# Performance work log

Measured on AMD Instinct MI355X. Metric: run time of the kernel, lower is better.

Reference implementation:

```python
import jax, jax.numpy as jnp
import numpy as np

B, S, H = 2, 2048, 1024
NH, NKV, HD = 16, 4, 64
G, R = NKV, NH // NKV  # 4 kv groups, 4 query heads per group


def setup_inputs() -> dict:
    key = jax.random.key(0)
    ks = jax.random.split(key, 7)
    scale = 1.0 / np.sqrt(H)
    return {
        "hidden_states": jax.random.normal(ks[0], (B, S, H), jnp.float32),
        "cos": jax.random.normal(ks[1], (S, HD), jnp.float32),
        "sin": jax.random.normal(ks[2], (S, HD), jnp.float32),
        "attention_mask": jnp.ones((B, S), jnp.float32),
        "Wq": jax.random.normal(ks[3], (H, NH * HD), jnp.float32) * scale,
        "Wk": jax.random.normal(ks[4], (H, NKV * HD), jnp.float32) * scale,
        "Wv": jax.random.normal(ks[5], (H, NKV * HD), jnp.float32) * scale,
        "Wo": jax.random.normal(ks[6], (NH * HD, H), jnp.float32) * scale,
    }


def _rotate_half(x):
    h = x.shape[-1] // 2
    return jnp.concatenate([-x[..., h:], x[..., :h]], axis=-1)


def reference(hidden_states, cos, sin, attention_mask, Wq, Wk, Wv, Wo):
    x = hidden_states
    q = (x @ Wq).reshape(B, S, NH, HD)
    k = (x @ Wk).reshape(B, S, NKV, HD)
    v = (x @ Wv).reshape(B, S, NKV, HD)
    # RoPE: cos/sin [S,HD] broadcast over batch and heads
    c = cos[None, :, None, :]
    s = sin[None, :, None, :]
    q = q * c + _rotate_half(q) * s
    k = k * c + _rotate_half(k) * s
    # GQA without materializing repeated KV: q grouped as [B,S,G,R,HD]
    qg = q.reshape(B, S, G, R, HD)
    scores = jnp.einsum("bsgrd,btgd->bgrst", qg, k) / np.sqrt(HD)  # [B,G,R,S,T]
    causal = jnp.tril(jnp.ones((S, S), bool))
    scores = jnp.where(causal[None, None, None], scores, -jnp.inf)
    scores = scores + ((1.0 - attention_mask) * -1e9)[:, None, None, None, :]
    probs = jax.nn.softmax(scores.astype(jnp.float32), axis=-1).astype(q.dtype)
    out = jnp.einsum("bgrst,btgd->bsgrd", probs, v).reshape(B, S, NH * HD)
    return out @ Wo
```

## Files before the change

### kernel.cpp

```cpp
#include <hip/hip_runtime.h>
#include <math.h>

#define B_   2
#define S_   2048
#define H_   1024
#define NH_  16
#define NKV_ 4
#define HD_  64
#define R_   (NH_ / NKV_)
#define QKVW 1536

typedef __attribute__((ext_vector_type(8))) short bf16x8;
typedef __attribute__((ext_vector_type(4))) float f32x4;

__device__ inline short f2bf(float f) {
    unsigned u = __float_as_uint(f);
    u += 0x7FFF + ((u >> 16) & 1);
    return (short)(u >> 16);
}

__device__ inline float exp2fast(float x) {
#if __has_builtin(__builtin_amdgcn_exp2f)
    return __builtin_amdgcn_exp2f(x);
#else
    float r; asm volatile("v_exp_f32 %0, %1\n\ts_nop 1" : "=v"(r) : "v"(x)); return r;
#endif
}

__device__ inline unsigned cvt_pk_bf16(float lo, float hi) {
    unsigned r;
    asm("v_cvt_pk_bf16_f32 %0, %1, %2" : "=v"(r) : "v"(lo), "v"(hi));
    return r;
}

#define LOG2E 1.4426950408889634f

__device__ inline void gload_lds16(const void* gptr, void* lptr) {
    __builtin_amdgcn_global_load_lds(
        (const __attribute__((address_space(1))) unsigned int*)gptr,
        (__attribute__((address_space(3))) unsigned int*)lptr,
        16, 0, 0);
}

__global__ __launch_bounds__(256) void tconv_all(const float* __restrict__ Wq,
                                                 const float* __restrict__ Wk,
                                                 const float* __restrict__ Wv,
                                                 const float* __restrict__ Wo,
                                                 short* __restrict__ Wqkvt,
                                                 short* __restrict__ Wot,
                                                 const float* __restrict__ x,
                                                 short* __restrict__ xb) {
    const int bx = blockIdx.x;
    const int tid = threadIdx.x;

    if (bx >= 640) {
        const size_t e0 = (size_t)(bx - 640) * 16384;
#pragma unroll
        for (int t = 0; t < 8; t++) {
            const size_t i = e0 + ((size_t)t * 256 + tid) * 8;
            float4 a = *(const float4*)&x[i];
            float4 c = *(const float4*)&x[i + 4];
            bf16x8 o;
            o[0] = f2bf(a.x); o[1] = f2bf(a.y); o[2] = f2bf(a.z); o[3] = f2bf(a.w);
            o[4] = f2bf(c.x); o[5] = f2bf(c.y); o[6] = f2bf(c.z); o[7] = f2bf(c.w);
            *(bf16x8*)&xb[i] = o;
        }
        return;
    }

    __shared__ short T[64][68];
    const float* W; short* Wt; int N, idx;
    if (bx < 256)      { W = Wq; Wt = Wqkvt;                     N = 1024; idx = bx; }
    else if (bx < 320) { W = Wk; Wt = Wqkvt + 1024 * 1024;       N = 256;  idx = bx - 256; }
    else if (bx < 384) { W = Wv; Wt = Wqkvt + 1280 * 1024;       N = 256;  idx = bx - 320; }
    else               { W = Wo; Wt = Wot;                       N = 1024; idx = bx - 384; }
    const int ntiles = N >> 6;
    const int n0 = (idx % ntiles) * 64;
    const int k0 = (idx / ntiles) * 64;

    const int r  = tid >> 4;
    const int c4 = (tid & 15) * 4;
#pragma unroll
    for (int t = 0; t < 4; t++) {
        int row = t * 16 + r;
        float4 v = *(const float4*)&W[(size_t)(k0 + row) * N + n0 + c4];
        T[c4 + 0][row] = f2bf(v.x);
        T[c4 + 1][row] = f2bf(v.y);
        T[c4 + 2][row] = f2bf(v.z);
        T[c4 + 3][row] = f2bf(v.w);
    }
    __syncthreads();
#pragma unroll
    for (int t = 0; t < 4; t++) {
        int row = t * 16 + r;
        short4 o = *(short4*)&T[row][c4];
        *(short4*)&Wt[(size_t)(n0 + row) * 1024 + k0 + c4] = o;
    }
}

__global__ __launch_bounds__(256) void gemm1_fused(const short* __restrict__ xb,
                                                   const short* __restrict__ Bt,
                                                   short* __restrict__ qkv,
                                                   short* __restrict__ Vtg,
                                                   const float* __restrict__ cosb,
                                                   const float* __restrict__ sinb) {
    __shared__ short Ah[64 * 32];
    __shared__ short Bh[128 * 32];

    const int tid  = threadIdx.x;
    const int w    = tid >> 6;
    const int lane = tid & 63;
    const int ln   = lane & 15;
    const int qd   = lane >> 4;
    const int wr   = w >> 1, wc = w & 1;
    const int row0 = blockIdx.y * 64;
    const int col0 = blockIdx.x * 128;

    const int sr = lane >> 2;
    const int sk = (lane & 3) * 8;

    f32x4 acc[2][4];
#pragma unroll
    for (int mi = 0; mi < 2; mi++)
#pragma unroll
        for (int ni = 0; ni < 4; ni++)
            acc[mi][ni] = (f32x4){0.f, 0.f, 0.f, 0.f};

    for (int k0 = 0; k0 < 1024; k0 += 32) {
        __syncthreads();
        gload_lds16(xb + (size_t)(row0 + w * 16 + sr) * 1024 + k0 + sk,      &Ah[(w * 16) * 32]);
        gload_lds16(Bt + (size_t)(col0 + w * 32 + sr) * 1024 + k0 + sk,      &Bh[(w * 32) * 32]);
        gload_lds16(Bt + (size_t)(col0 + w * 32 + 16 + sr) * 1024 + k0 + sk, &Bh[(w * 32 + 16) * 32]);
        __syncthreads();

        bf16x8 af[2], bfr[4];
#pragma unroll
        for (int mi = 0; mi < 2; mi++)
            af[mi] = *(const bf16x8*)&Ah[(wr * 32 + mi * 16 + ln) * 32 + qd * 8];
#pragma unroll
        for (int ni = 0; ni < 4; ni++)
            bfr[ni] = *(const bf16x8*)&Bh[(wc * 64 + ni * 16 + ln) * 32 + qd * 8];
#pragma unroll
        for (int mi = 0; mi < 2; mi++)
#pragma unroll
            for (int ni = 0; ni < 4; ni++)
                acc[mi][ni] = __builtin_amdgcn_mfma_f32_16x16x32_bf16(af[mi], bfr[ni], acc[mi][ni], 0, 0, 0);
    }

    const int colw = col0 + wc * 64;
    if (colw < H_ + NKV_ * HD_) {
#pragma unroll
        for (int mi = 0; mi < 2; mi++)
#pragma unroll
            for (int i = 0; i < 4; i++) {
                const int row  = row0 + wr * 32 + mi * 16 + qd * 4 + i;
                const int spos = row & (S_ - 1);
                const float* cp = cosb + (size_t)spos * HD_;
                const float* sp = sinb + (size_t)spos * HD_;
                float o0[4];
#pragma unroll
                for (int ni = 0; ni < 2; ni++) {
                    const int d = ni * 16 + ln;
                    float x0 = acc[mi][ni][i], x1 = acc[mi][ni + 2][i];
                    o0[ni]     = x0 * cp[d]      - x1 * sp[d];
                    o0[ni + 2] = x1 * cp[d + 32] + x0 * sp[d + 32];
                }
                short* Cp = qkv + (size_t)row * QKVW + colw + ln;
#pragma unroll
                for (int ni = 0; ni < 4; ni++) Cp[ni * 16] = f2bf(o0[ni]);
            }
    } else {
        const int g = (colw - (H_ + NKV_ * HD_)) >> 6;
#pragma unroll
        for (int mi = 0; mi < 2; mi++) {
            const int rbase = row0 + wr * 32 + mi * 16 + qd * 4;
            const int bg = ((rbase >> 11) * NKV_) + g;
            const int s0 = rbase & (S_ - 1);
#pragma unroll
            for (int ni = 0; ni < 4; ni++) {
                const int d = ni * 16 + ln;
                short4 pk = { f2bf(acc[mi][ni][0]), f2bf(acc[mi][ni][1]),
                              f2bf(acc[mi][ni][2]), f2bf(acc[mi][ni][3]) };
                *(short4*)&Vtg[((size_t)bg * HD_ + d) * S_ + s0] = pk;
            }
        }
    }
}

__global__ __launch_bounds__(256) void gemm2_bt(const short* __restrict__ A, int lda,
                                                const short* __restrict__ Bt,
                                                float* __restrict__ C, int ldc,
                                                int K) {
    __shared__ short Ah[64 * 32];
    __shared__ short Bh[128 * 32];

    const int tid  = threadIdx.x;
    const int w    = tid >> 6;
    const int lane = tid & 63;
    const int ln   = lane & 15;
    const int qd   = lane >> 4;
    const int wr   = w >> 1, wc = w & 1;
    const int row0 = blockIdx.y * 64;
    const int col0 = blockIdx.x * 128;

    const int sr = lane >> 2;
    const int sk = (lane & 3) * 8;

    f32x4 acc[2][4];
#pragma unroll
    for (int mi = 0; mi < 2; mi++)
#pragma unroll
        for (int ni = 0; ni < 4; ni++)
            acc[mi][ni] = (f32x4){0.f, 0.f, 0.f, 0.f};

    for (int k0 = 0; k0 < K; k0 += 32) {
        __syncthreads();
        gload_lds16(A + (size_t)(row0 + w * 16 + sr) * lda + k0 + sk, &Ah[(w * 16) * 32]);
        gload_lds16(Bt + (size_t)(col0 + w * 32 + sr) * K + k0 + sk, &Bh[(w * 32) * 32]);
        gload_lds16(Bt + (size_t)(col0 + w * 32 + 16 + sr) * K + k0 + sk, &Bh[(w * 32 + 16) * 32]);
        __syncthreads();

        bf16x8 af[2], bfr[4];
#pragma unroll
        for (int mi = 0; mi < 2; mi++)
            af[mi] = *(const bf16x8*)&Ah[(wr * 32 + mi * 16 + ln) * 32 + qd * 8];
#pragma unroll
        for (int ni = 0; ni < 4; ni++)
            bfr[ni] = *(const bf16x8*)&Bh[(wc * 64 + ni * 16 + ln) * 32 + qd * 8];
#pragma unroll
        for (int mi = 0; mi < 2; mi++)
#pragma unroll
            for (int ni = 0; ni < 4; ni++)
                acc[mi][ni] = __builtin_amdgcn_mfma_f32_16x16x32_bf16(af[mi], bfr[ni], acc[mi][ni], 0, 0, 0);
    }

#pragma unroll
    for (int mi = 0; mi < 2; mi++)
#pragma unroll
        for (int i = 0; i < 4; i++) {
            const size_t row = row0 + wr * 32 + mi * 16 + qd * 4 + i;
            float* Cp = C + row * ldc + col0 + wc * 64 + ln;
#pragma unroll
            for (int ni = 0; ni < 4; ni++) Cp[ni * 16] = acc[mi][ni][i];
        }
}

__global__ __launch_bounds__(512, 2) void attn_kernel(short* __restrict__ qkv,
                                                      const short* __restrict__ Vtg,
                                                      const float* __restrict__ maskb) {
    const int tid  = threadIdx.x;
    const int w    = tid >> 6;
    const int lane = tid & 63;
    const int ln   = lane & 15;
    const int qd   = lane >> 4;

    const int fid = blockIdx.x;
    const int bg  = fid & 7;
    const int u   = fid >> 3;
    const int b   = bg >> 2;
    const int g   = bg & 3;
    const int h   = g * R_ + (u & 3);
    const int a   = u >> 2;

    __shared__ short Ks[2][64 * 72];
    __shared__ short Vt[2][64 * 72];
    __shared__ short Ps[8][16 * 72];
    __shared__ float mskS[2][64];
    short* const ps = Ps[w];

    const short* const Kb = qkv + (size_t)b * S_ * QKVW + H_ + g * HD_;
    const short* const Vb = Vtg + (size_t)bg * HD_ * S_;
    const float* const mb = maskb + b * S_;

    const int fr = tid >> 3;
    const int fc = (tid & 7) * 8;

#pragma unroll 1
    for (int ph = 0; ph < 2; ph++) {
        const int qt   = ph ? (15 - a) : a;
        const int rowb = qt * 128 + w * 16;
        const int ktd  = 2 * qt + (w >> 2);
        const int ntp  = 2 * qt + 2;
        const int qrow = rowb + ln;

        bf16x8 qf0, qf1;
        {
            const short* qp = qkv + (size_t)(b * S_ + rowb + ln) * QKVW + h * HD_;
            qf0 = *(const bf16x8*)&qp[qd * 8];
            qf1 = *(const bf16x8*)&qp[32 + qd * 8];
        }

        f32x4 O[4] = {};
        float mrow = -1e30f, lrow = 0.0f;

        *(bf16x8*)&Ks[0][fr * 72 + fc] = *(const bf16x8*)&Kb[(size_t)fr * QKVW + fc];
        *(bf16x8*)&Vt[0][fr * 72 + fc] = *(const bf16x8*)&Vb[(size_t)fr * S_ + fc];
        if (tid < 64) mskS[0][tid] = (1.0f - mb[tid]) * (-1e9f * LOG2E);
        __syncthreads();

        int cur = 0;
#pragma unroll 1
        for (int kt = 0; kt < ntp; kt++) {
            const int base = kt * 64;
            const bool pf = (kt + 1 < ntp);

            bf16x8 pk, pv;
            float pm = 0.0f;
            if (pf) {
                const int nb = base + 64;
                pk = *(const bf16x8*)&Kb[(size_t)(nb + fr) * QKVW + fc];
                pv = *(const bf16x8*)&Vb[(size_t)fr * S_ + nb + fc];
                if (tid < 64) pm = (1.0f - mb[nb + tid]) * (-1e9f * LOG2E);
            }

            if (kt <= ktd) {
                f32x4 St[4];
#pragma unroll
                for (int kg = 0; kg < 4; kg++) {
                    bf16x8 ka0 = *(const bf16x8*)&Ks[cur][(kg * 16 + ln) * 72 + qd * 8];
                    bf16x8 ka1 = *(const bf16x8*)&Ks[cur][(kg * 16 + ln) * 72 + 32 + qd * 8];
                    f32x4 z = {0.f, 0.f, 0.f, 0.f};
                    z = __builtin_amdgcn_mfma_f32_16x16x32_bf16(ka0, qf0, z, 0, 0, 0);
                    St[kg] = __builtin_amdgcn_mfma_f32_16x16x32_bf16(ka1, qf1, z, 0, 0, 0);
                }

                bf16x8 vb[2][4];
#pragma unroll
                for (int kc2 = 0; kc2 < 2; kc2++)
#pragma unroll
                    for (int dt = 0; dt < 4; dt++)
                        vb[kc2][dt] = *(const bf16x8*)&Vt[cur][(dt * 16 + ln) * 72 + kc2 * 32 + qd * 8];

                float sc[4][4];
#pragma unroll
                for (int kg = 0; kg < 4; kg++) {
                    float4 mv = *(const float4*)&mskS[cur][kg * 16 + qd * 4];
                    sc[kg][0] = fmaf(St[kg][0], 0.125f * LOG2E, mv.x);
                    sc[kg][1] = fmaf(St[kg][1], 0.125f * LOG2E, mv.y);
                    sc[kg][2] = fmaf(St[kg][2], 0.125f * LOG2E, mv.z);
                    sc[kg][3] = fmaf(St[kg][3], 0.125f * LOG2E, mv.w);
                }
                if (kt == ktd) {
#pragma unroll
                    for (int kg = 0; kg < 4; kg++) {
                        const int keyb = base + kg * 16 + qd * 4;
#pragma unroll
                        for (int i = 0; i < 4; i++)
                            if (keyb + i > qrow) sc[kg][i] = -1e30f;
                    }
                }

                float mx = sc[0][0];
#pragma unroll
                for (int kg = 0; kg < 4; kg++)
#pragma unroll
                    for (int i = 0; i < 4; i++) mx = fmaxf(mx, sc[kg][i]);
                mx = fmaxf(mx, __shfl_xor(mx, 16));
                mx = fmaxf(mx, __shfl_xor(mx, 32));

                if (__ballot(mx > mrow + 11.5416f)) {
                    float nm    = fmaxf(mrow, mx);
                    float alpha = exp2fast(mrow - nm);
                    lrow *= alpha;
#pragma unroll
                    for (int i = 0; i < 4; i++) {
                        float av = __shfl(alpha, qd * 4 + i);
#pragma unroll
                        for (int dt = 0; dt < 4; dt++) O[dt][i] *= av;
                    }
                    mrow = nm;
                }
                const float nm = mrow;

                float ls = 0.0f;
#pragma unroll
                for (int kg = 0; kg < 4; kg++)
#pragma unroll
                    for (int i = 0; i < 4; i++) {
                        float p = exp2fast(sc[kg][i] - nm);
                        sc[kg][i] = p;
                        ls += p;
                    }
                ls += __shfl_xor(ls, 16);
                ls += __shfl_xor(ls, 32);
                lrow += ls;

#pragma unroll
                for (int kg = 0; kg < 4; kg++) {
                    uint2 pw;
                    pw.x = cvt_pk_bf16(sc[kg][0], sc[kg][1]);
                    pw.y = cvt_pk_bf16(sc[kg][2], sc[kg][3]);
                    *(uint2*)&ps[ln * 72 + kg * 16 + qd * 4] = pw;
                }

#pragma unroll
                for (int kc2 = 0; kc2 < 2; kc2++) {
                    bf16x8 pa = *(const bf16x8*)&ps[ln * 72 + kc2 * 32 + qd * 8];
#pragma unroll
                    for (int dt = 0; dt < 4; dt++)
                        O[dt] = __builtin_amdgcn_mfma_f32_16x16x32_bf16(pa, vb[kc2][dt], O[dt], 0, 0, 0);
                }
            }

            if (pf) {
                const int nxt = cur ^ 1;
                *(bf16x8*)&Ks[nxt][fr * 72 + fc] = pk;
                *(bf16x8*)&Vt[nxt][fr * 72 + fc] = pv;
                if (tid < 64) mskS[nxt][tid] = pm;
            }
            __syncthreads();
            cur ^= 1;
        }

#pragma unroll
        for (int i = 0; i < 4; i++) {
            float li  = __shfl(lrow, qd * 4 + i);
            float inv = 1.0f / li;
            const int row = rowb + qd * 4 + i;
            short* op = qkv + (size_t)(b * S_ + row) * QKVW + h * HD_ + ln;
#pragma unroll
            for (int dt = 0; dt < 4; dt++) op[dt * 16] = f2bf(O[dt][i] * inv);
        }
    }
}

extern "C" void kernel_launch(void* const* d_in, const int* in_sizes, int n_in,
                              void* d_out, int out_size, void* d_ws, size_t ws_size,
                              hipStream_t stream) {
    const float* x     = (const float*)d_in[0];
    const float* cosb  = (const float*)d_in[1];
    const float* sinb  = (const float*)d_in[2];
    const float* maskb = (const float*)d_in[3];
    const float* Wq    = (const float*)d_in[4];
    const float* Wk    = (const float*)d_in[5];
    const float* Wv    = (const float*)d_in[6];
    const float* Wo    = (const float*)d_in[7];

    const int M = B_ * S_;

    short* qkv   = (short*)d_ws;
    short* Wqkvt = qkv + (size_t)M * QKVW;
    short* Wot   = Wqkvt + (size_t)QKVW * H_;
    short* Vtg   = Wot + (size_t)H_ * H_;
    short* xb    = (short*)d_out;
    float* out   = (float*)d_out;

    dim3 blk(256);

    tconv_all<<<dim3(896), blk, 0, stream>>>(Wq, Wk, Wv, Wo, Wqkvt, Wot, x, xb);

    gemm1_fused<<<dim3(QKVW / 128, M / 64), blk, 0, stream>>>(xb, Wqkvt, qkv, Vtg, cosb, sinb);

    attn_kernel<<<dim3(256), dim3(512), 0, stream>>>(qkv, Vtg, maskb);

    gemm2_bt<<<dim3(H_ / 128, M / 64), blk, 0, stream>>>(qkv, QKVW, Wot, out, H_, H_);
}
```

Measured before the change: 184.4 us.

## Fuse all stages into one cooperative persistent kernel with grid syncs

Replaces the four launches (weight/activation conversion, QKV GEMM with RoPE, attention, output GEMM) with one cooperative kernel of 256 persistent blocks of 512 threads. Grid-wide syncs separate the stages. The x-to-bf16 conversion is folded into the first GEMM's A-tile load, and both GEMMs now double-buffer their LDS tiles. This removes launch gaps and the separate xb pass. In exchange, each stage is limited to 256 blocks at one block per CU, the GEMM tiles are smaller per wave, and the grid syncs add their own cost.

Result: slower. 496.1 us (+169.1%).

```diff
diff --git a/kernel.cpp b/kernel.cpp
--- a/kernel.cpp
+++ b/kernel.cpp
@@ -1,5 +1,8 @@
 #include <hip/hip_runtime.h>
+#include <hip/hip_cooperative_groups.h>
 #include <math.h>
+
+namespace cg = cooperative_groups;
 
 #define B_   2
 #define S_   2048
@@ -42,384 +45,368 @@
         16, 0, 0);
 }
 
-__global__ __launch_bounds__(256) void tconv_all(const float* __restrict__ Wq,
-                                                 const float* __restrict__ Wk,
-                                                 const float* __restrict__ Wv,
-                                                 const float* __restrict__ Wo,
-                                                 short* __restrict__ Wqkvt,
-                                                 short* __restrict__ Wot,
-                                                 const float* __restrict__ x,
-                                                 short* __restrict__ xb) {
-    const int bx = blockIdx.x;
-    const int tid = threadIdx.x;
-
-    if (bx >= 640) {
-        const size_t e0 = (size_t)(bx - 640) * 16384;
-#pragma unroll
-        for (int t = 0; t < 8; t++) {
-            const size_t i = e0 + ((size_t)t * 256 + tid) * 8;
-            float4 a = *(const float4*)&x[i];
-            float4 c = *(const float4*)&x[i + 4];
-            bf16x8 o;
-            o[0] = f2bf(a.x); o[1] = f2bf(a.y); o[2] = f2bf(a.z); o[3] = f2bf(a.w);
-            o[4] = f2bf(c.x); o[5] = f2bf(c.y); o[6] = f2bf(c.z); o[7] = f2bf(c.w);
-            *(bf16x8*)&xb[i] = o;
-        }
-        return;
-    }
-
-    __shared__ short T[64][68];
-    const float* W; short* Wt; int N, idx;
-    if (bx < 256)      { W = Wq; Wt = Wqkvt;                     N = 1024; idx = bx; }
-    else if (bx < 320) { W = Wk; Wt = Wqkvt + 1024 * 1024;       N = 256;  idx = bx - 256; }
-    else if (bx < 384) { W = Wv; Wt = Wqkvt + 1280 * 1024;       N = 256;  idx = bx - 320; }
-    else               { W = Wo; Wt = Wot;                       N = 1024; idx = bx - 384; }
-    const int ntiles = N >> 6;
-    const int n0 = (idx % ntiles) * 64;
-    const int k0 = (idx / ntiles) * 64;
-
-    const int r  = tid >> 4;
-    const int c4 = (tid & 15) * 4;
-#pragma unroll
-    for (int t = 0; t < 4; t++) {
-        int row = t * 16 + r;
-        float4 v = *(const float4*)&W[(size_t)(k0 + row) * N + n0 + c4];
-        T[c4 + 0][row] = f2bf(v.x);
-        T[c4 + 1][row] = f2bf(v.y);
-        T[c4 + 2][row] = f2bf(v.z);
-        T[c4 + 3][row] = f2bf(v.w);
-    }
-    __syncthreads();
-#pragma unroll
-    for (int t = 0; t < 4; t++) {
-        int row = t * 16 + r;
-        short4 o = *(short4*)&T[row][c4];
-        *(short4*)&Wt[(size_t)(n0 + row) * 1024 + k0 + c4] = o;
-    }
-}
-
-__global__ __launch_bounds__(256) void gemm1_fused(const short* __restrict__ xb,
-                                                   const short* __restrict__ Bt,
-                                                   short* __restrict__ qkv,
-                                                   short* __restrict__ Vtg,
-                                                   const float* __restrict__ cosb,
-                                                   const float* __restrict__ sinb) {
-    __shared__ short Ah[64 * 32];
-    __shared__ short Bh[128 * 32];
+__global__ __launch_bounds__(512, 1) void mega(const float* __restrict__ x,
+                                               const float* __restrict__ cosb,
+                                               const float* __restrict__ sinb,
+                                               const float* __restrict__ maskb,
+                                               const float* __restrict__ Wq,
+                                               const float* __restrict__ Wk,
+                                               const float* __restrict__ Wv,
+                                               const float* __restrict__ Wo,
+                                               short* __restrict__ qkv,
+                                               short* __restrict__ Wqkvt,
+                                               short* __restrict__ Wot,
+                                               short* __restrict__ Vtg,
+                                               float* __restrict__ out) {
+    cg::grid_group grid = cg::this_grid();
+
+    __shared__ union {
+        struct { short T[64][68]; } tc;
+        struct { short Ah[2][64 * 32]; short Bh[2][128 * 32]; } g;
+        struct { short Ks[2][64 * 72]; short Vt[2][64 * 72];
+                 short Ps[8][16 * 72]; float mskS[2][64]; } at;
+    } sm;
 
     const int tid  = threadIdx.x;
+    const int bid  = blockIdx.x;
     const int w    = tid >> 6;
     const int lane = tid & 63;
     const int ln   = lane & 15;
     const int qd   = lane >> 4;
-    const int wr   = w >> 1, wc = w & 1;
-    const int row0 = blockIdx.y * 64;
-    const int col0 = blockIdx.x * 128;
-
-    const int sr = lane >> 2;
-    const int sk = (lane & 3) * 8;
-
-    f32x4 acc[2][4];
-#pragma unroll
-    for (int mi = 0; mi < 2; mi++)
-#pragma unroll
-        for (int ni = 0; ni < 4; ni++)
-            acc[mi][ni] = (f32x4){0.f, 0.f, 0.f, 0.f};
-
-    for (int k0 = 0; k0 < 1024; k0 += 32) {
-        __syncthreads();
-        gload_lds16(xb + (size_t)(row0 + w * 16 + sr) * 1024 + k0 + sk,      &Ah[(w * 16) * 32]);
-        gload_lds16(Bt + (size_t)(col0 + w * 32 + sr) * 1024 + k0 + sk,      &Bh[(w * 32) * 32]);
-        gload_lds16(Bt + (size_t)(col0 + w * 32 + 16 + sr) * 1024 + k0 + sk, &Bh[(w * 32 + 16) * 32]);
-        __syncthreads();
-
-        bf16x8 af[2], bfr[4];
-#pragma unroll
-        for (int mi = 0; mi < 2; mi++)
-            af[mi] = *(const bf16x8*)&Ah[(wr * 32 + mi * 16 + ln) * 32 + qd * 8];
-#pragma unroll
-        for (int ni = 0; ni < 4; ni++)
-            bfr[ni] = *(const bf16x8*)&Bh[(wc * 64 + ni * 16 + ln) * 32 + qd * 8];
-#pragma unroll
-        for (int mi = 0; mi < 2; mi++)
-#pragma unroll
-            for (int ni = 0; ni < 4; ni++)
-                acc[mi][ni] = __builtin_amdgcn_mfma_f32_16x16x32_bf16(af[mi], bfr[ni], acc[mi][ni], 0, 0, 0);
-    }
-
-    const int colw = col0 + wc * 64;
-    if (colw < H_ + NKV_ * HD_) {
-#pragma unroll
-        for (int mi = 0; mi < 2; mi++)
-#pragma unroll
-            for (int i = 0; i < 4; i++) {
-                const int row  = row0 + wr * 32 + mi * 16 + qd * 4 + i;
-                const int spos = row & (S_ - 1);
-                const float* cp = cosb + (size_t)spos * HD_;
-                const float* sp = sinb + (size_t)spos * HD_;
-                float o0[4];
-#pragma unroll
-                for (int ni = 0; ni < 2; ni++) {
-                    const int d = ni * 16 + ln;
-                    float x0 = acc[mi][ni][i], x1 = acc[mi][ni + 2][i];
-                    o0[ni]     = x0 * cp[d]      - x1 * sp[d];
-                    o0[ni + 2] = x1 * cp[d + 32] + x0 * sp[d + 32];
-                }
-                short* Cp = qkv + (size_t)row * QKVW + colw + ln;
-#pragma unroll
-                for (int ni = 0; ni < 4; ni++) Cp[ni * 16] = f2bf(o0[ni]);
-            }
-    } else {
-        const int g = (colw - (H_ + NKV_ * HD_)) >> 6;
-#pragma unroll
-        for (int mi = 0; mi < 2; mi++) {
-            const int rbase = row0 + wr * 32 + mi * 16 + qd * 4;
-            const int bg = ((rbase >> 11) * NKV_) + g;
-            const int s0 = rbase & (S_ - 1);
-#pragma unroll
-            for (int ni = 0; ni < 4; ni++) {
-                const int d = ni * 16 + ln;
-                short4 pk = { f2bf(acc[mi][ni][0]), f2bf(acc[mi][ni][1]),
-                              f2bf(acc[mi][ni][2]), f2bf(acc[mi][ni][3]) };
-                *(short4*)&Vtg[((size_t)bg * HD_ + d) * S_ + s0] = pk;
+
+    {
+        const int r  = tid >> 4;
+        const int c4 = (tid & 15) * 4;
+        for (int bx = bid; bx < 640; bx += 256) {
+            const float* W; short* Wt; int N, idx;
+            if (bx < 256)      { W = Wq; Wt = Wqkvt;               N = 1024; idx = bx; }
+            else if (bx < 320) { W = Wk; Wt = Wqkvt + 1024 * 1024; N = 256;  idx = bx - 256; }
+            else if (bx < 384) { W = Wv; Wt = Wqkvt + 1280 * 1024; N = 256;  idx = bx - 320; }
+            else               { W = Wo; Wt = Wot;                 N = 1024; idx = bx - 384; }
+            const int ntiles = N >> 6;
+            const int n0 = (idx % ntiles) * 64;
+            const int k0 = (idx / ntiles) * 64;
+
+            __syncthreads();
+#pragma unroll
+            for (int t = 0; t < 2; t++) {
+                int row = t * 32 + r;
+                float4 v = *(const float4*)&W[(size_t)(k0 + row) * N + n0 + c4];
+                sm.tc.T[c4 + 0][row] = f2bf(v.x);
+                sm.tc.T[c4 + 1][row] = f2bf(v.y);
+                sm.tc.T[c4 + 2][row] = f2bf(v.z);
+                sm.tc.T[c4 + 3][row] = f2bf(v.w);
+            }
+            __syncthreads();
+#pragma unroll
+            for (int t = 0; t < 2; t++) {
+                int row = t * 32 + r;
+                short4 o = *(short4*)&sm.tc.T[row][c4];
+                *(short4*)&Wt[(size_t)(n0 + row) * 1024 + k0 + c4] = o;
             }
         }
     }
-}
-
-__global__ __launch_bounds__(256) void gemm2_bt(const short* __restrict__ A, int lda,
-                                                const short* __restrict__ Bt,
-                                                float* __restrict__ C, int ldc,
-                                                int K) {
-    __shared__ short Ah[64 * 32];
-    __shared__ short Bh[128 * 32];
-
-    const int tid  = threadIdx.x;
-    const int w    = tid >> 6;
-    const int lane = tid & 63;
-    const int ln   = lane & 15;
-    const int qd   = lane >> 4;
-    const int wr   = w >> 1, wc = w & 1;
-    const int row0 = blockIdx.y * 64;
-    const int col0 = blockIdx.x * 128;
-
-    const int sr = lane >> 2;
-    const int sk = (lane & 3) * 8;
-
-    f32x4 acc[2][4];
-#pragma unroll
-    for (int mi = 0; mi < 2; mi++)
-#pragma unroll
-        for (int ni = 0; ni < 4; ni++)
-            acc[mi][ni] = (f32x4){0.f, 0.f, 0.f, 0.f};
-
-    for (int k0 = 0; k0 < K; k0 += 32) {
-        __syncthreads();
-        gload_lds16(A + (size_t)(row0 + w * 16 + sr) * lda + k0 + sk, &Ah[(w * 16) * 32]);
-        gload_lds16(Bt + (size_t)(col0 + w * 32 + sr) * K + k0 + sk, &Bh[(w * 32) * 32]);
-        gload_lds16(Bt + (size_t)(col0 + w * 32 + 16 + sr) * K + k0 + sk, &Bh[(w * 32 + 16) * 32]);
-        __syncthreads();
-
-        bf16x8 af[2], bfr[4];
-#pragma unroll
-        for (int mi = 0; mi < 2; mi++)
-            af[mi] = *(const bf16x8*)&Ah[(wr * 32 + mi * 16 + ln) * 32 + qd * 8];
-#pragma unroll
-        for (int ni = 0; ni < 4; ni++)
-            bfr[ni] = *(const bf16x8*)&Bh[(wc * 64 + ni * 16 + ln) * 32 + qd * 8];
-#pragma unroll
-        for (int mi = 0; mi < 2; mi++)
-#pragma unroll
-            for (int ni = 0; ni < 4; ni++)
-                acc[mi][ni] = __builtin_amdgcn_mfma_f32_16x16x32_bf16(af[mi], bfr[ni], acc[mi][ni], 0, 0, 0);
+    grid.sync();
+
+    {
+        const int wr = w >> 1;
+        const int wc = w & 1;
+        const int sr = lane >> 2, sk = (lane & 3) * 8;
+        const int ar  = tid >> 3;
+        const int ac4 = (tid & 7) * 4;
+
+        for (int tile = bid; tile < 768; tile += 256) {
+            const int row0 = (tile / 12) * 64;
+            const int col0 = (tile % 12) * 128;
+
+            f32x4 acc[4];
+#pragma unroll
+            for (int ni = 0; ni < 4; ni++) acc[ni] = (f32x4){0.f, 0.f, 0.f, 0.f};
+
+            const float* xp = x + (size_t)(row0 + ar) * 1024 + ac4;
+            const short* bp = Wqkvt + (size_t)(col0 + w * 16 + sr) * 1024 + sk;
+
+            {
+                float4 a1 = *(const float4*)xp;
+                short4 o = { f2bf(a1.x), f2bf(a1.y), f2bf(a1.z), f2bf(a1.w) };
+                *(short4*)&sm.g.Ah[0][ar * 32 + ac4] = o;
+            }
+            gload_lds16(bp, &sm.g.Bh[0][(w * 16) * 32]);
+            __syncthreads();
+
+            for (int t = 0; t < 32; t++) {
+                const int cur = t & 1, nxt = cur ^ 1;
+                if (t + 1 < 32) {
+                    const int k1 = (t + 1) * 32;
+                    gload_lds16(bp + k1, &sm.g.Bh[nxt][(w * 16) * 32]);
+                    float4 a1 = *(const float4*)(xp + k1);
+                    short4 o = { f2bf(a1.x), f2bf(a1.y), f2bf(a1.z), f2bf(a1.w) };
+                    *(short4*)&sm.g.Ah[nxt][ar * 32 + ac4] = o;
+                }
+                bf16x8 af = *(const bf16x8*)&sm.g.Ah[cur][(wr * 16 + ln) * 32 + qd * 8];
+                bf16x8 bfr[4];
+#pragma unroll
+                for (int ni = 0; ni < 4; ni++)
+                    bfr[ni] = *(const bf16x8*)&sm.g.Bh[cur][(wc * 64 + ni * 16 + ln) * 32 + qd * 8];
+#pragma unroll
+                for (int ni = 0; ni < 4; ni++)
+                    acc[ni] = __builtin_amdgcn_mfma_f32_16x16x32_bf16(af, bfr[ni], acc[ni], 0, 0, 0);
+                __syncthreads();
+            }
+
+            const int colw = col0 + wc * 64;
+            if (colw < H_ + NKV_ * HD_) {
+#pragma unroll
+                for (int i = 0; i < 4; i++) {
+                    const int row  = row0 + wr * 16 + qd * 4 + i;
+                    const int spos = row & (S_ - 1);
+                    const float* cp = cosb + (size_t)spos * HD_;
+                    const float* sp = sinb + (size_t)spos * HD_;
+                    float o0[4];
+#pragma unroll
+                    for (int ni = 0; ni < 2; ni++) {
+                        const int d = ni * 16 + ln;
+                        float x0 = acc[ni][i], x1 = acc[ni + 2][i];
+                        o0[ni]     = x0 * cp[d]      - x1 * sp[d];
+                        o0[ni + 2] = x1 * cp[d + 32] + x0 * sp[d + 32];
+                    }
+                    short* Cp = qkv + (size_t)row * QKVW + colw + ln;
+#pragma unroll
+                    for (int ni = 0; ni < 4; ni++) Cp[ni * 16] = f2bf(o0[ni]);
+                }
+            } else {
+                const int g2 = (colw - (H_ + NKV_ * HD_)) >> 6;
+                const int rbase = row0 + wr * 16 + qd * 4;
+                const int bg2 = ((rbase >> 11) * NKV_) + g2;
+                const int s0 = rbase & (S_ - 1);
+#pragma unroll
+                for (int ni = 0; ni < 4; ni++) {
+                    const int d = ni * 16 + ln;
+                    short4 pk = { f2bf(acc[ni][0]), f2bf(acc[ni][1]),
+                                  f2bf(acc[ni][2]), f2bf(acc[ni][3]) };
+                    *(short4*)&Vtg[((size_t)bg2 * HD_ + d) * S_ + s0] = pk;
+                }
+            }
+            __syncthreads();
+        }
     }
-
-#pragma unroll
-    for (int mi = 0; mi < 2; mi++)
-#pragma unroll
-        for (int i = 0; i < 4; i++) {
-            const size_t row = row0 + wr * 32 + mi * 16 + qd * 4 + i;
-            float* Cp = C + row * ldc + col0 + wc * 64 + ln;
-#pragma unroll
-            for (int ni = 0; ni < 4; ni++) Cp[ni * 16] = acc[mi][ni][i];
+    grid.sync();
+
+    {
+        const int fid = bid;
+        const int bg  = fid & 7;
+        const int u   = fid >> 3;
+        const int b   = bg >> 2;
+        const int g   = bg & 3;
+        const int h   = g * R_ + (u & 3);
+        const int a   = u >> 2;
+
+        short* const ps = sm.at.Ps[w];
+
+        const short* const Kb = qkv + (size_t)b * S_ * QKVW + H_ + g * HD_;
+        const short* const Vb = Vtg + (size_t)bg * HD_ * S_;
+        const float* const mb = maskb + b * S_;
+
+        const int fr = tid >> 3;
+        const int fc = (tid & 7) * 8;
+
+#pragma unroll 1
+        for (int ph = 0; ph < 2; ph++) {
+            const int qt   = ph ? (15 - a) : a;
+            const int rowb = qt * 128 + w * 16;
+            const int ktd  = 2 * qt + (w >> 2);
+            const int ntp  = 2 * qt + 2;
+            const int qrow = rowb + ln;
+
+            bf16x8 qf0, qf1;
+            {
+                const short* qp = qkv + (size_t)(b * S_ + rowb + ln) * QKVW + h * HD_;
+                qf0 = *(const bf16x8*)&qp[qd * 8];
+                qf1 = *(const bf16x8*)&qp[32 + qd * 8];
+            }
+
+            f32x4 O[4] = {};
+            float mrow = -1e30f, lrow = 0.0f;
+
+            __syncthreads();
+            *(bf16x8*)&sm.at.Ks[0][fr * 72 + fc] = *(const bf16x8*)&Kb[(size_t)fr * QKVW + fc];
+            *(bf16x8*)&sm.at.Vt[0][fr * 72 + fc] = *(const bf16x8*)&Vb[(size_t)fr * S_ + fc];
+            if (tid < 64) sm.at.mskS[0][tid] = (1.0f - mb[tid]) * (-1e9f * LOG2E);
+            __syncthreads();
+
+            int cur = 0;
+#pragma unroll 1
+            for (int kt = 0; kt < ntp; kt++) {
+                const int base = kt * 64;
+                const bool pf = (kt + 1 < ntp);
+
+                bf16x8 pk, pv;
+                float pm = 0.0f;
+                if (pf) {
+                    const int nb = base + 64;
+                    pk = *(const bf16x8*)&Kb[(size_t)(nb + fr) * QKVW + fc];
+                    pv = *(const bf16x8*)&Vb[(size_t)fr * S_ + nb + fc];
+                    if (tid < 64) pm = (1.0f - mb[nb + tid]) * (-1e9f * LOG2E);
+                }
+
+                if (kt <= ktd) {
+                    f32x4 St[4];
+#pragma unroll
+                    for (int kg = 0; kg < 4; kg++) {
+                        bf16x8 ka0 = *(const bf16x8*)&sm.at.Ks[cur][(kg * 16 + ln) * 72 + qd * 8];
+                        bf16x8 ka1 = *(const bf16x8*)&sm.at.Ks[cur][(kg * 16 + ln) * 72 + 32 + qd * 8];
+                        f32x4 z = {0.f, 0.f, 0.f, 0.f};
+                        z = __builtin_amdgcn_mfma_f32_16x16x32_bf16(ka0, qf0, z, 0, 0, 0);
+                        St[kg] = __builtin_amdgcn_mfma_f32_16x16x32_bf16(ka1, qf1, z, 0, 0, 0);
+                    }
+
+                    bf16x8 vb[2][4];
+#pragma unroll
+                    for (int kc2 = 0; kc2 < 2; kc2++)
+#pragma unroll
+                        for (int dt = 0; dt < 4; dt++)
+                            vb[kc2][dt] = *(const bf16x8*)&sm.at.Vt[cur][(dt * 16 + ln) * 72 + kc2 * 32 + qd * 8];
+
+                    float sc[4][4];
+#pragma unroll
+                    for (int kg = 0; kg < 4; kg++) {
+                        float4 mv = *(const float4*)&sm.at.mskS[cur][kg * 16 + qd * 4];
+                        sc[kg][0] = fmaf(St[kg][0], 0.125f * LOG2E, mv.x);
+                        sc[kg][1] = fmaf(St[kg][1], 0.125f * LOG2E, mv.y);
+                        sc[kg][2] = fmaf(St[kg][2], 0.125f * LOG2E, mv.z);
+                        sc[kg][3] = fmaf(St[kg][3], 0.125f * LOG2E, mv.w);
+                    }
+                    if (kt == ktd) {
+#pragma unroll
+                        for (int kg = 0; kg < 4; kg++) {
+                            const int keyb = base + kg * 16 + qd * 4;
+#pragma unroll
+                            for (int i = 0; i < 4; i++)
+                                if (keyb + i > qrow) sc[kg][i] = -1e30f;
+                        }
+                    }
+
+                    float mx = sc[0][0];
+#pragma unroll
+                    for (int kg = 0; kg < 4; kg++)
+#pragma unroll
+                        for (int i = 0; i < 4; i++) mx = fmaxf(mx, sc[kg][i]);
+                    mx = fmaxf(mx, __shfl_xor(mx, 16));
+                    mx = fmaxf(mx, __shfl_xor(mx, 32));
+
+                    if (__ballot(mx > mrow + 11.5416f)) {
+                        float nm    = fmaxf(mrow, mx);
+                        float alpha = exp2fast(mrow - nm);
+                        lrow *= alpha;
+#pragma unroll
+                        for (int i = 0; i < 4; i++) {
+                            float av = __shfl(alpha, qd * 4 + i);
+#pragma unroll
+                            for (int dt = 0; dt < 4; dt++) O[dt][i] *= av;
+                        }
+                        mrow = nm;
+                    }
+                    const float nm = mrow;
+
+                    float ls = 0.0f;
+#pragma unroll
+                    for (int kg = 0; kg < 4; kg++)
+#pragma unroll
+                        for (int i = 0; i < 4; i++) {
+                            float p = exp2fast(sc[kg][i] - nm);
+                            sc[kg][i] = p;
+                            ls += p;
+                        }
+                    ls += __shfl_xor(ls, 16);
+                    ls += __shfl_xor(ls, 32);
+                    lrow += ls;
+
+#pragma unroll
+                    for (int kg = 0; kg < 4; kg++) {
+                        uint2 pw;
+                        pw.x = cvt_pk_bf16(sc[kg][0], sc[kg][1]);
+                        pw.y = cvt_pk_bf16(sc[kg][2], sc[kg][3]);
+                        *(uint2*)&ps[ln * 72 + kg * 16 + qd * 4] = pw;
+                    }
+
+#pragma unroll
+                    for (int kc2 = 0; kc2 < 2; kc2++) {
+                        bf16x8 pa = *(const bf16x8*)&ps[ln * 72 + kc2 * 32 + qd * 8];
+#pragma unroll
+                        for (int dt = 0; dt < 4; dt++)
+                            O[dt] = __builtin_amdgcn_mfma_f32_16x16x32_bf16(pa, vb[kc2][dt], O[dt], 0, 0, 0);
+                    }
+                }
+
+                if (pf) {
+                    const int nxt = cur ^ 1;
+                    *(bf16x8*)&sm.at.Ks[nxt][fr * 72 + fc] = pk;
+                    *(bf16x8*)&sm.at.Vt[nxt][fr * 72 + fc] = pv;
+                    if (tid < 64) sm.at.mskS[nxt][tid] = pm;
+                }
+                __syncthreads();
+                cur ^= 1;
+            }
+
+#pragma unroll
+            for (int i = 0; i < 4; i++) {
+                float li  = __shfl(lrow, qd * 4 + i);
+                float inv = 1.0f / li;
+                const int row = rowb + qd * 4 + i;
+                short* op = qkv + (size_t)(b * S_ + row) * QKVW + h * HD_ + ln;
+#pragma unroll
+                for (int dt = 0; dt < 4; dt++) op[dt * 16] = f2bf(O[dt][i] * inv);
+            }
         }
-}
-
-__global__ __launch_bounds__(512, 2) void attn_kernel(short* __restrict__ qkv,
-                                                      const short* __restrict__ Vtg,
-                                                      const float* __restrict__ maskb) {
-    const int tid  = threadIdx.x;
-    const int w    = tid >> 6;
-    const int lane = tid & 63;
-    const int ln   = lane & 15;
-    const int qd   = lane >> 4;
-
-    const int fid = blockIdx.x;
-    const int bg  = fid & 7;
-    const int u   = fid >> 3;
-    const int b   = bg >> 2;
-    const int g   = bg & 3;
-    const int h   = g * R_ + (u & 3);
-    const int a   = u >> 2;
-
-    __shared__ short Ks[2][64 * 72];
-    __shared__ short Vt[2][64 * 72];
-    __shared__ short Ps[8][16 * 72];
-    __shared__ float mskS[2][64];
-    short* const ps = Ps[w];
-
-    const short* const Kb = qkv + (size_t)b * S_ * QKVW + H_ + g * HD_;
-    const short* const Vb = Vtg + (size_t)bg * HD_ * S_;
-    const float* const mb = maskb + b * S_;
-
-    const int fr = tid >> 3;
-    const int fc = (tid & 7) * 8;
-
-#pragma unroll 1
-    for (int ph = 0; ph < 2; ph++) {
-        const int qt   = ph ? (15 - a) : a;
-        const int rowb = qt * 128 + w * 16;
-        const int ktd  = 2 * qt + (w >> 2);
-        const int ntp  = 2 * qt + 2;
-        const int qrow = rowb + ln;
-
-        bf16x8 qf0, qf1;
-        {
-            const short* qp = qkv + (size_t)(b * S_ + rowb + ln) * QKVW + h * HD_;
-            qf0 = *(const bf16x8*)&qp[qd * 8];
-            qf1 = *(const bf16x8*)&qp[32 + qd * 8];
-        }
-
-        f32x4 O[4] = {};
-        float mrow = -1e30f, lrow = 0.0f;
-
-        *(bf16x8*)&Ks[0][fr * 72 + fc] = *(const bf16x8*)&Kb[(size_t)fr * QKVW + fc];
-        *(bf16x8*)&Vt[0][fr * 72 + fc] = *(const bf16x8*)&Vb[(size_t)fr * S_ + fc];
-        if (tid < 64) mskS[0][tid] = (1.0f - mb[tid]) * (-1e9f * LOG2E);
-        __syncthreads();
-
-        int cur = 0;
-#pragma unroll 1
-        for (int kt = 0; kt < ntp; kt++) {
-            const int base = kt * 64;
-            const bool pf = (kt + 1 < ntp);
-
-            bf16x8 pk, pv;
-            float pm = 0.0f;
-            if (pf) {
-                const int nb = base + 64;
-                pk = *(const bf16x8*)&Kb[(size_t)(nb + fr) * QKVW + fc];
-                pv = *(const bf16x8*)&Vb[(size_t)fr * S_ + nb + fc];
-                if (tid < 64) pm = (1.0f - mb[nb + tid]) * (-1e9f * LOG2E);
-            }
-
-            if (kt <= ktd) {
-                f32x4 St[4];
-#pragma unroll
-                for (int kg = 0; kg < 4; kg++) {
-                    bf16x8 ka0 = *(const bf16x8*)&Ks[cur][(kg * 16 + ln) * 72 + qd * 8];
-                    bf16x8 ka1 = *(const bf16x8*)&Ks[cur][(kg * 16 + ln) * 72 + 32 + qd * 8];
-                    f32x4 z = {0.f, 0.f, 0.f, 0.f};
-                    z = __builtin_amdgcn_mfma_f32_16x16x32_bf16(ka0, qf0, z, 0, 0, 0);
-                    St[kg] = __builtin_amdgcn_mfma_f32_16x16x32_bf16(ka1, qf1, z, 0, 0, 0);
-                }
-
-                bf16x8 vb[2][4];
-#pragma unroll
-                for (int kc2 = 0; kc2 < 2; kc2++)
-#pragma unroll
-                    for (int dt = 0; dt < 4; dt++)
-                        vb[kc2][dt] = *(const bf16x8*)&Vt[cur][(dt * 16 + ln) * 72 + kc2 * 32 + qd * 8];
-
-                float sc[4][4];
-#pragma unroll
-                for (int kg = 0; kg < 4; kg++) {
-                    float4 mv = *(const float4*)&mskS[cur][kg * 16 + qd * 4];
-                    sc[kg][0] = fmaf(St[kg][0], 0.125f * LOG2E, mv.x);
-                    sc[kg][1] = fmaf(St[kg][1], 0.125f * LOG2E, mv.y);
-                    sc[kg][2] = fmaf(St[kg][2], 0.125f * LOG2E, mv.z);
-                    sc[kg][3] = fmaf(St[kg][3], 0.125f * LOG2E, mv.w);
-                }
-                if (kt == ktd) {
-#pragma unroll
-                    for (int kg = 0; kg < 4; kg++) {
-                        const int keyb = base + kg * 16 + qd * 4;
-#pragma unroll
-                        for (int i = 0; i < 4; i++)
-                            if (keyb + i > qrow) sc[kg][i] = -1e30f;
-                    }
-                }
-
-                float mx = sc[0][0];
-#pragma unroll
-                for (int kg = 0; kg < 4; kg++)
-#pragma unroll
-                    for (int i = 0; i < 4; i++) mx = fmaxf(mx, sc[kg][i]);
-                mx = fmaxf(mx, __shfl_xor(mx, 16));
-                mx = fmaxf(mx, __shfl_xor(mx, 32));
-
-                if (__ballot(mx > mrow + 11.5416f)) {
-                    float nm    = fmaxf(mrow, mx);
-                    float alpha = exp2fast(mrow - nm);
-                    lrow *= alpha;
-#pragma unroll
-                    for (int i = 0; i < 4; i++) {
-                        float av = __shfl(alpha, qd * 4 + i);
-#pragma unroll
-                        for (int dt = 0; dt < 4; dt++) O[dt][i] *= av;
-                    }
-                    mrow = nm;
-                }
-                const float nm = mrow;
-
-                float ls = 0.0f;
-#pragma unroll
-                for (int kg = 0; kg < 4; kg++)
-#pragma unroll
-                    for (int i = 0; i < 4; i++) {
-                        float p = exp2fast(sc[kg][i] - nm);
-                        sc[kg][i] = p;
-                        ls += p;
-                    }
-                ls += __shfl_xor(ls, 16);
-                ls += __shfl_xor(ls, 32);
-                lrow += ls;
-
-#pragma unroll
-                for (int kg = 0; kg < 4; kg++) {
-                    uint2 pw;
-                    pw.x = cvt_pk_bf16(sc[kg][0], sc[kg][1]);
-                    pw.y = cvt_pk_bf16(sc[kg][2], sc[kg][3]);
-                    *(uint2*)&ps[ln * 72 + kg * 16 + qd * 4] = pw;
-                }
-
-#pragma unroll
-                for (int kc2 = 0; kc2 < 2; kc2++) {
-                    bf16x8 pa = *(const bf16x8*)&ps[ln * 72 + kc2 * 32 + qd * 8];
-#pragma unroll
-                    for (int dt = 0; dt < 4; dt++)
-                        O[dt] = __builtin_amdgcn_mfma_f32_16x16x32_bf16(pa, vb[kc2][dt], O[dt], 0, 0, 0);
-                }
-            }
-
-            if (pf) {
-                const int nxt = cur ^ 1;
-                *(bf16x8*)&Ks[nxt][fr * 72 + fc] = pk;
-                *(bf16x8*)&Vt[nxt][fr * 72 + fc] = pv;
-                if (tid < 64) mskS[nxt][tid] = pm;
-            }
-            __syncthreads();
-            cur ^= 1;
-        }
-
-#pragma unroll
-        for (int i = 0; i < 4; i++) {
-            float li  = __shfl(lrow, qd * 4 + i);
-            float inv = 1.0f / li;
-            const int row = rowb + qd * 4 + i;
-            short* op = qkv + (size_t)(b * S_ + row) * QKVW + h * HD_ + ln;
-#pragma unroll
-            for (int dt = 0; dt < 4; dt++) op[dt * 16] = f2bf(O[dt][i] * inv);
+    }
+    grid.sync();
+
+    {
+        const int wr = w >> 1;
+        const int wc = w & 1;
+        const int sr = lane >> 2, sk = (lane & 3) * 8;
+
+        for (int tile = bid; tile < 512; tile += 256) {
+            const int row0 = (tile / 8) * 64;
+            const int col0 = (tile % 8) * 128;
+
+            f32x4 acc[4];
+#pragma unroll
+            for (int ni = 0; ni < 4; ni++) acc[ni] = (f32x4){0.f, 0.f, 0.f, 0.f};
+
+            const short* ap = qkv + (size_t)(row0 + (w & 3) * 16 + sr) * QKVW + sk;
+            const short* bp = Wot + (size_t)(col0 + w * 16 + sr) * 1024 + sk;
+
+            if (w < 4) gload_lds16(ap, &sm.g.Ah[0][((w & 3) * 16) * 32]);
+            gload_lds16(bp, &sm.g.Bh[0][(w * 16) * 32]);
+            __syncthreads();
+
+            for (int t = 0; t < 32; t++) {
+                const int cur = t & 1, nxt = cur ^ 1;
+                if (t + 1 < 32) {
+                    const int k1 = (t + 1) * 32;
+                    if (w < 4) gload_lds16(ap + k1, &sm.g.Ah[nxt][((w & 3) * 16) * 32]);
+                    gload_lds16(bp + k1, &sm.g.Bh[nxt][(w * 16) * 32]);
+                }
+                bf16x8 af = *(const bf16x8*)&sm.g.Ah[cur][(wr * 16 + ln) * 32 + qd * 8];
+                bf16x8 bfr[4];
+#pragma unroll
+                for (int ni = 0; ni < 4; ni++)
+                    bfr[ni] = *(const bf16x8*)&sm.g.Bh[cur][(wc * 64 + ni * 16 + ln) * 32 + qd * 8];
+#pragma unroll
+                for (int ni = 0; ni < 4; ni++)
+                    acc[ni] = __builtin_amdgcn_mfma_f32_16x16x32_bf16(af, bfr[ni], acc[ni], 0, 0, 0);
+                __syncthreads();
+            }
+
+#pragma unroll
+            for (int i = 0; i < 4; i++) {
+                const size_t row = row0 + wr * 16 + qd * 4 + i;
+                float* Cp = out + row * 1024 + col0 + wc * 64 + ln;
+#pragma unroll
+                for (int ni = 0; ni < 4; ni++) Cp[ni * 16] = acc[ni][i];
+            }
+            __syncthreads();
         }
     }
 }
@@ -442,16 +429,13 @@
     short* Wqkvt = qkv + (size_t)M * QKVW;
     short* Wot   = Wqkvt + (size_t)QKVW * H_;
     short* Vtg   = Wot + (size_t)H_ * H_;
-    short* xb    = (short*)d_out;
     float* out   = (float*)d_out;
 
-    dim3 blk(256);
-
-    tconv_all<<<dim3(896), blk, 0, stream>>>(Wq, Wk, Wv, Wo, Wqkvt, Wot, x, xb);
-
-    gemm1_fused<<<dim3(QKVW / 128, M / 64), blk, 0, stream>>>(xb, Wqkvt, qkv, Vtg, cosb, sinb);
-
-    attn_kernel<<<dim3(256), dim3(512), 0, stream>>>(qkv, Vtg, maskb);
-
-    gemm2_bt<<<dim3(H_ / 128, M / 64), blk, 0, stream>>>(qkv, QKVW, Wot, out, H_, H_);
-}
+    void* args[] = { (void*)&x, (void*)&cosb, (void*)&sinb, (void*)&maskb,
+                     (void*)&Wq, (void*)&Wk, (void*)&Wv, (void*)&Wo,
+                     (void*)&qkv, (void*)&Wqkvt, (void*)&Wot, (void*)&Vtg,
+                     (void*)&out };
+
+    hipLaunchCooperativeKernel((const void*)mega, dim3(256), dim3(512),
+                               args, 0, stream);
+}
```
